# Optimization experiments

Measured on AMD Instinct MI355X. Metric: run time of the kernel, lower is better.

The kernel has to match this reference:

```python
import jax, jax.numpy as jnp
import numpy as np

GRID_SIZE = 8
POS_LAMBDA = 1.0
POS_MARGIN = 1.0
NEG_MARGIN = 0.2
LOSS_LAMBDA = 1.0

N, C, HR, WR = 4, 256, 60, 60
H, W = HR * GRID_SIZE, WR * GRID_SIZE


def setup_inputs() -> dict:
    key = jax.random.key(0)
    k1, k2, k3 = jax.random.split(key, 3)
    desc1 = jax.random.normal(k1, (N, C, HR, WR), dtype=jnp.float32)
    desc2 = jax.random.normal(k2, (N, C, HR, WR), dtype=jnp.float32)
    # near-identity homographies to keep the perspective divide well-conditioned
    noise = jax.random.normal(k3, (N, 3, 3), dtype=jnp.float32) * 0.01
    homo21 = jnp.eye(3, dtype=jnp.float32)[None] + noise
    vis_mask1 = jnp.ones((N, 1, H, W), dtype=jnp.float32)
    return {"desc1": desc1, "desc2": desc2, "homo21": homo21, "vis_mask1": vis_mask1}


def reference(desc1, desc2, homo21, vis_mask1):
    n, c, hr, wr = desc1.shape
    gs = GRID_SIZE
    dt = desc1.dtype
    # cell-center coordinate grid, (x, y) order: hr x wr x 2
    ys, xs = jnp.meshgrid(jnp.arange(hr, dtype=dt), jnp.arange(wr, dtype=dt), indexing="ij")
    grid = jnp.stack([xs, ys], axis=-1) * gs + gs // 2
    grid = jnp.broadcast_to(grid[None], (n, hr, wr, 2))
    # warp grid by homography: n x hr x wr x 2
    pts = jnp.concatenate([grid, jnp.ones((n, hr, wr, 1), dtype=dt)], axis=-1)
    wpts = jnp.einsum("nij,nhwj->nhwi", homo21, pts)
    w_grid = wpts[..., :2] / wpts[..., 2:3]
    # all-pairs distance between grid (dims 1,2) and warped grid (dims 3,4)
    diff = grid[:, :, :, None, None, :] - w_grid[:, None, None, :, :, :]
    grid_dist = jnp.linalg.norm(diff, axis=-1)  # n,hr,wr,hr,wr
    s = (grid_dist <= gs - 0.5).astype(dt)
    ns = 1.0 - s
    # space_to_depth(vis_mask1, gs).prod(dim=1): product over each gs x gs block
    vm = vis_mask1[:, 0].reshape(n, hr, gs, wr, gs).prod(axis=(2, 4))  # n,hr,wr
    vm = vm.reshape(n, 1, 1, hr, wr)
    s = s * vm
    ns = ns * vm
    # all-pairs descriptor dot product: n,hr,wr,hr,wr
    dot_desc = jnp.einsum("nchw,ncij->nhwij", desc1, desc2)
    pos_dist = jnp.maximum(POS_MARGIN - dot_desc, 0.0)
    neg_dist = jnp.maximum(dot_desc - NEG_MARGIN, 0.0)
    loss = POS_LAMBDA * s * pos_dist + ns * neg_dist
    norm = hr * wr * vm.sum()
    return loss.sum() / norm * LOSS_LAMBDA
```

## Files before the change

### kernel.cpp

```cpp
#include <hip/hip_runtime.h>
#include <stdint.h>

#define NB   4
#define CC   256
#define WR   60
#define MM   3600
#define HH   480
#define WW   480
#define GS   8
#define MT   29
#define NBLK (MT * MT * NB)
#define PREPB 57

typedef float f32x4  __attribute__((ext_vector_type(4)));
typedef float f32x16 __attribute__((ext_vector_type(16)));
typedef int   i32x8  __attribute__((ext_vector_type(8)));

__global__ __launch_bounds__(256) void pack_prep(
    const float* __restrict__ d1, const float* __restrict__ d2,
    const float* __restrict__ homo, const float* __restrict__ vis,
    unsigned char* __restrict__ p1, unsigned char* __restrict__ p2,
    float2* __restrict__ wg, float* __restrict__ vmarr,
    float* __restrict__ vm_part) {
  __shared__ float vmred[4];
  int kt = blockIdx.x;
  int mtile = blockIdx.y;
  int z = blockIdx.z;
  int bid = kt + 4 * (mtile + MT * z);
  int b = z & 3;
  const float* src = ((z >> 2) ? d2 : d1) + (size_t)b * CC * MM;
  unsigned char* dstbase = ((z >> 2) ? p2 : p1) + (size_t)(b * MT + mtile) * 32768;
  int tid = threadIdx.x;
  int t = tid >> 6, lane = tid & 63;
  int r = lane & 31, hi = lane >> 5;
  int m = mtile * 128 + t * 32 + r;
  int c0 = kt * 64 + hi * 32;

  unsigned int ww[8];
  if (m < MM) {
    const float* s0 = src + (size_t)c0 * MM + m;
#pragma unroll
    for (int d = 0; d < 8; ++d) {
      float f0 = s0[(size_t)(4 * d + 0) * MM];
      float f1 = s0[(size_t)(4 * d + 1) * MM];
      float f2 = s0[(size_t)(4 * d + 2) * MM];
      float f3 = s0[(size_t)(4 * d + 3) * MM];
      unsigned int wv = __builtin_amdgcn_cvt_pk_fp8_f32(f0, f1, 0, false);
      wv = __builtin_amdgcn_cvt_pk_fp8_f32(f2, f3, wv, true);
      ww[d] = wv;
    }
  } else {
#pragma unroll
    for (int d = 0; d < 8; ++d) ww[d] = 0;
  }
  uint4* dst = (uint4*)(dstbase + (size_t)(kt * 4 + t) * 2048 + lane * 32);
  dst[0] = make_uint4(ww[0], ww[1], ww[2], ww[3]);
  dst[1] = make_uint4(ww[4], ww[5], ww[6], ww[7]);

  if (bid < PREPB) {
    int idx = bid * 256 + tid;
    float p = 0.f;
    if (idx < NB * MM) {
      int bb = idx / MM, cell = idx - bb * MM;
      int h1 = cell / WR, w1 = cell - h1 * WR;
      float gx = (float)(w1 * GS + GS / 2);
      float gy = (float)(h1 * GS + GS / 2);
      const float* Hm = homo + bb * 9;
      float X = Hm[0] * gx + Hm[1] * gy + Hm[2];
      float Y = Hm[3] * gx + Hm[4] * gy + Hm[5];
      float Z = Hm[6] * gx + Hm[7] * gy + Hm[8];
      wg[idx] = make_float2(X / Z, Y / Z);
      const float* v = vis + (size_t)bb * HH * WW + (size_t)(h1 * GS) * WW + w1 * GS;
      float prod = 1.f;
#pragma unroll
      for (int rr = 0; rr < GS; ++rr) {
        const float4* rp = (const float4*)(v + (size_t)rr * WW);
        float4 a = rp[0], c = rp[1];
        prod *= a.x * a.y * a.z * a.w;
        prod *= c.x * c.y * c.z * c.w;
      }
      vmarr[idx] = prod;
      p = prod;
    }
#pragma unroll
    for (int off = 32; off; off >>= 1) p += __shfl_down(p, off, 64);
    if ((tid & 63) == 0) vmred[tid >> 6] = p;
    __syncthreads();
    if (tid == 0)
      vm_part[bid] = vmred[0] + vmred[1] + vmred[2] + vmred[3];
  }
}

__global__ __launch_bounds__(256, 2) void hinge_gemm(
    const unsigned char* __restrict__ Ap, const unsigned char* __restrict__ Bp,
    const float2* __restrict__ wg, const float* __restrict__ vmarr,
    float* __restrict__ block_part) {
  __shared__ float partial[4];

  int orig = blockIdx.x + MT * blockIdx.y + MT * MT * blockIdx.z;
  const int q = NBLK >> 3, rmod = NBLK & 7;
  int xcd = orig & 7, loc = orig >> 3;
  int wgid = (xcd < rmod ? xcd * (q + 1) : rmod * (q + 1) + (xcd - rmod) * q) + loc;
  int b = wgid / (MT * MT);
  int rem = wgid - b * (MT * MT);
  int mtile = rem / MT;
  int ntile = rem - mtile * MT;

  int tid = threadIdx.x, lane = tid & 63, w = tid >> 6;
  int colL = lane & 31, hi = lane >> 5;
  int wave_m = w >> 1, wave_n = w & 1;

  const char* Af = (const char*)Ap + (size_t)(b * MT + mtile) * 32768
                   + (size_t)(wave_m * 2) * 2048 + lane * 32;
  const char* Bf = (const char*)Bp + (size_t)(b * MT + ntile) * 32768
                   + (size_t)(wave_n * 2) * 2048 + lane * 32;

  f32x16 acc[2][2];
#pragma unroll
  for (int i = 0; i < 2; ++i)
#pragma unroll
    for (int j = 0; j < 2; ++j)
#pragma unroll
      for (int k = 0; k < 16; ++k) acc[i][j][k] = 0.f;

  i32x8 a0[2], b0[2], a1[2], b1[2];
#pragma unroll
  for (int t2 = 0; t2 < 2; ++t2) {
    a0[t2] = *(const i32x8*)(Af + t2 * 2048);
    b0[t2] = *(const i32x8*)(Bf + t2 * 2048);
  }

#pragma unroll
  for (int kt = 0; kt < 4; ++kt) {
    if (kt < 3) {
      const char* an = Af + (kt + 1) * 8192;
      const char* bn = Bf + (kt + 1) * 8192;
#pragma unroll
      for (int t2 = 0; t2 < 2; ++t2) {
        a1[t2] = *(const i32x8*)(an + t2 * 2048);
        b1[t2] = *(const i32x8*)(bn + t2 * 2048);
      }
    }
#pragma unroll
    for (int mi = 0; mi < 2; ++mi)
#pragma unroll
      for (int ni = 0; ni < 2; ++ni)
        acc[mi][ni] = __builtin_amdgcn_mfma_scale_f32_32x32x64_f8f6f4(
            a0[mi], b0[ni], acc[mi][ni], 0, 0,
            0, 127, 0, 127 );
#pragma unroll
    for (int t2 = 0; t2 < 2; ++t2) { a0[t2] = a1[t2]; b0[t2] = b1[t2]; }
  }

  float gxv[32], gyv[32];
#pragma unroll
  for (int mi = 0; mi < 2; ++mi)
#pragma unroll
    for (int reg = 0; reg < 16; ++reg) {
      int gm = mtile * 128 + wave_m * 64 + mi * 32 + (reg & 3) + 8 * (reg >> 2) + 4 * hi;
      float gmf = (float)gm;
      float h1 = floorf(fmaf(gmf, (1.0f / 60.0f), (1.0f / 120.0f)));
      float w1 = fmaf(h1, -60.f, gmf);
      gxv[mi * 16 + reg] = fmaf(w1, 8.f, 4.f);
      gyv[mi * 16 + reg] = fmaf(h1, 8.f, 4.f);
    }

  float sum = 0.f;
  const float2* wgb = wg + (size_t)b * MM;
  const float*  vmb = vmarr + (size_t)b * MM;
#pragma unroll
  for (int ni = 0; ni < 2; ++ni) {
    int gn = ntile * 128 + wave_n * 64 + ni * 32 + colL;
    bool nok = gn < MM;
    float2 wgv = nok ? wgb[gn] : make_float2(1e9f, 1e9f);
    float  vmv = nok ? vmb[gn] : 0.f;
#pragma unroll
    for (int mi = 0; mi < 2; ++mi)
#pragma unroll
      for (int reg = 0; reg < 16; ++reg) {
        float dot = acc[mi][ni][reg];
        float dx = gxv[mi * 16 + reg] - wgv.x;
        float dy = gyv[mi * 16 + reg] - wgv.y;
        float d2 = fmaf(dx, dx, dy * dy);
        float a = (d2 <= 56.25f) ? (1.0f - dot) : (dot - 0.2f);
        sum = fmaf(vmv, fmaxf(a, 0.f), sum);
      }
  }
#pragma unroll
  for (int off = 32; off; off >>= 1) sum += __shfl_down(sum, off, 64);
  if (lane == 0) partial[w] = sum;
  __syncthreads();
  if (tid == 0) {
    int fbid = ntile + MT * (mtile + MT * b);
    block_part[fbid] = partial[0] + partial[1] + partial[2] + partial[3];
  }
}

__global__ __launch_bounds__(256) void finalize_k(
    const float* __restrict__ block_part, const float* __restrict__ vm_part,
    float* __restrict__ out) {
  __shared__ float red[8];
  int tid = threadIdx.x;
  float s = 0.f, v = 0.f;
  for (int i = tid; i < NBLK; i += 256) s += block_part[i];
  if (tid < PREPB) v = vm_part[tid];
#pragma unroll
  for (int off = 32; off; off >>= 1) {
    s += __shfl_down(s, off, 64);
    v += __shfl_down(v, off, 64);
  }
  if ((tid & 63) == 0) { red[tid >> 6] = s; red[4 + (tid >> 6)] = v; }
  __syncthreads();
  if (tid == 0) {
    float S = red[0] + red[1] + red[2] + red[3];
    float V = red[4] + red[5] + red[6] + red[7];
    out[0] = S / ((float)MM * V);
  }
}

extern "C" void kernel_launch(void* const* d_in, const int* in_sizes, int n_in,
                              void* d_out, int out_size, void* d_ws, size_t ws_size,
                              hipStream_t stream) {
  const float* desc1 = (const float*)d_in[0];
  const float* desc2 = (const float*)d_in[1];
  const float* homo  = (const float*)d_in[2];
  const float* vis   = (const float*)d_in[3];
  float* out = (float*)d_out;

  char* ws = (char*)d_ws;
  unsigned char* Ap = (unsigned char*)ws;
  unsigned char* Bp = (unsigned char*)(ws + 3801088);
  float2* wg         = (float2*)(ws + 7602176);
  float*  vm         = (float*) (ws + 7717376);
  float*  vm_part    = (float*) (ws + 7774976);
  float*  block_part = (float*) (ws + 7775232);

  dim3 pgrid(4, MT, 2 * NB);
  pack_prep<<<pgrid, 256, 0, stream>>>(desc1, desc2, homo, vis, Ap, Bp,
                                       wg, vm, vm_part);

  dim3 ggrid(MT, MT, NB);
  hinge_gemm<<<ggrid, 256, 0, stream>>>(Ap, Bp, wg, vm, block_part);

  finalize_k<<<1, 256, 0, stream>>>(block_part, vm_part, out);
}
```

Before: 114.6 us.

## Fuse finalize into GEMM via atomics and last-block reduction, raise occupancy

Removes the separate finalize kernel: the GEMM blocks and prep blocks atomically add their partial sums into a small accumulator, and the last GEMM block (found with an atomic counter) writes the final loss. This saves one kernel launch, at the cost of a memset before the work. The epilogue is also restructured to compute grid coordinates inline instead of holding 64-element arrays, which lowers register pressure, and launch bounds are raised to 3 blocks per CU. The risks are atomic contention on a single address and a float summation order that is no longer deterministic.

Measured after the change: 173.8 us. 1.52x slower.

```diff
diff --git a/kernel.cpp b/kernel.cpp
--- a/kernel.cpp
+++ b/kernel.cpp
@@ -21,7 +21,7 @@
     const float* __restrict__ homo, const float* __restrict__ vis,
     unsigned char* __restrict__ p1, unsigned char* __restrict__ p2,
     float2* __restrict__ wg, float* __restrict__ vmarr,
-    float* __restrict__ vm_part) {
+    float* __restrict__ acc_sv) {
   __shared__ float vmred[4];
   int kt = blockIdx.x;
   int mtile = blockIdx.y;
@@ -87,14 +87,14 @@
     if ((tid & 63) == 0) vmred[tid >> 6] = p;
     __syncthreads();
     if (tid == 0)
-      vm_part[bid] = vmred[0] + vmred[1] + vmred[2] + vmred[3];
+      atomicAdd(&acc_sv[1], vmred[0] + vmred[1] + vmred[2] + vmred[3]);
   }
 }
 
-__global__ __launch_bounds__(256, 2) void hinge_gemm(
+__global__ __launch_bounds__(256, 3) void hinge_gemm(
     const unsigned char* __restrict__ Ap, const unsigned char* __restrict__ Bp,
     const float2* __restrict__ wg, const float* __restrict__ vmarr,
-    float* __restrict__ block_part) {
+    float* __restrict__ acc_sv, float* __restrict__ out) {
   __shared__ float partial[4];
 
   int orig = blockIdx.x + MT * blockIdx.y + MT * MT * blockIdx.z;
@@ -152,7 +152,19 @@
     for (int t2 = 0; t2 < 2; ++t2) { a0[t2] = a1[t2]; b0[t2] = b1[t2]; }
   }
 
-  float gxv[32], gyv[32];
+  float wx[2], wy[2], vv[2];
+  const float2* wgb = wg + (size_t)b * MM;
+  const float*  vmb = vmarr + (size_t)b * MM;
+#pragma unroll
+  for (int ni = 0; ni < 2; ++ni) {
+    int gn = ntile * 128 + wave_n * 64 + ni * 32 + colL;
+    bool nok = gn < MM;
+    float2 wgv = nok ? wgb[gn] : make_float2(1e9f, 1e9f);
+    wx[ni] = wgv.x; wy[ni] = wgv.y;
+    vv[ni] = nok ? vmb[gn] : 0.f;
+  }
+
+  float sum = 0.f;
 #pragma unroll
   for (int mi = 0; mi < 2; ++mi)
 #pragma unroll
@@ -161,60 +173,31 @@
       float gmf = (float)gm;
       float h1 = floorf(fmaf(gmf, (1.0f / 60.0f), (1.0f / 120.0f)));
       float w1 = fmaf(h1, -60.f, gmf);
-      gxv[mi * 16 + reg] = fmaf(w1, 8.f, 4.f);
-      gyv[mi * 16 + reg] = fmaf(h1, 8.f, 4.f);
-    }
-
-  float sum = 0.f;
-  const float2* wgb = wg + (size_t)b * MM;
-  const float*  vmb = vmarr + (size_t)b * MM;
-#pragma unroll
-  for (int ni = 0; ni < 2; ++ni) {
-    int gn = ntile * 128 + wave_n * 64 + ni * 32 + colL;
-    bool nok = gn < MM;
-    float2 wgv = nok ? wgb[gn] : make_float2(1e9f, 1e9f);
-    float  vmv = nok ? vmb[gn] : 0.f;
-#pragma unroll
-    for (int mi = 0; mi < 2; ++mi)
-#pragma unroll
-      for (int reg = 0; reg < 16; ++reg) {
+      float gx = fmaf(w1, 8.f, 4.f);
+      float gy = fmaf(h1, 8.f, 4.f);
+#pragma unroll
+      for (int ni = 0; ni < 2; ++ni) {
         float dot = acc[mi][ni][reg];
-        float dx = gxv[mi * 16 + reg] - wgv.x;
-        float dy = gyv[mi * 16 + reg] - wgv.y;
+        float dx = gx - wx[ni];
+        float dy = gy - wy[ni];
         float d2 = fmaf(dx, dx, dy * dy);
         float a = (d2 <= 56.25f) ? (1.0f - dot) : (dot - 0.2f);
-        sum = fmaf(vmv, fmaxf(a, 0.f), sum);
+        sum = fmaf(vv[ni], fmaxf(a, 0.f), sum);
       }
-  }
+    }
 #pragma unroll
   for (int off = 32; off; off >>= 1) sum += __shfl_down(sum, off, 64);
   if (lane == 0) partial[w] = sum;
   __syncthreads();
   if (tid == 0) {
-    int fbid = ntile + MT * (mtile + MT * b);
-    block_part[fbid] = partial[0] + partial[1] + partial[2] + partial[3];
-  }
-}
-
-__global__ __launch_bounds__(256) void finalize_k(
-    const float* __restrict__ block_part, const float* __restrict__ vm_part,
-    float* __restrict__ out) {
-  __shared__ float red[8];
-  int tid = threadIdx.x;
-  float s = 0.f, v = 0.f;
-  for (int i = tid; i < NBLK; i += 256) s += block_part[i];
-  if (tid < PREPB) v = vm_part[tid];
-#pragma unroll
-  for (int off = 32; off; off >>= 1) {
-    s += __shfl_down(s, off, 64);
-    v += __shfl_down(v, off, 64);
-  }
-  if ((tid & 63) == 0) { red[tid >> 6] = s; red[4 + (tid >> 6)] = v; }
-  __syncthreads();
-  if (tid == 0) {
-    float S = red[0] + red[1] + red[2] + red[3];
-    float V = red[4] + red[5] + red[6] + red[7];
-    out[0] = S / ((float)MM * V);
+    atomicAdd(&acc_sv[0], partial[0] + partial[1] + partial[2] + partial[3]);
+    __threadfence();
+    unsigned old = atomicAdd((unsigned*)&acc_sv[2], 1u);
+    if (old == (unsigned)(NBLK - 1)) {
+      float S = atomicAdd(&acc_sv[0], 0.f);
+      float V = atomicAdd(&acc_sv[1], 0.f);
+      out[0] = S / ((float)MM * V);
+    }
   }
 }
 
@@ -230,17 +213,16 @@
   char* ws = (char*)d_ws;
   unsigned char* Ap = (unsigned char*)ws;
   unsigned char* Bp = (unsigned char*)(ws + 3801088);
-  float2* wg         = (float2*)(ws + 7602176);
-  float*  vm         = (float*) (ws + 7717376);
-  float*  vm_part    = (float*) (ws + 7774976);
-  float*  block_part = (float*) (ws + 7775232);
+  float2* wg      = (float2*)(ws + 7602176);
+  float*  vm      = (float*) (ws + 7717376);
+  float*  acc_sv  = (float*) (ws + 7774976);
+
+  hipMemsetAsync(acc_sv, 0, 12, stream);
 
   dim3 pgrid(4, MT, 2 * NB);
   pack_prep<<<pgrid, 256, 0, stream>>>(desc1, desc2, homo, vis, Ap, Bp,
-                                       wg, vm, vm_part);
+                                       wg, vm, acc_sv);
 
   dim3 ggrid(MT, MT, NB);
-  hinge_gemm<<<ggrid, 256, 0, stream>>>(Ap, Bp, wg, vm, block_part);
-
-  finalize_k<<<1, 256, 0, stream>>>(block_part, vm_part, out);
+  hinge_gemm<<<ggrid, 256, 0, stream>>>(Ap, Bp, wg, vm, acc_sv, out);
 }
```
